# Optimization experiments

Hardware: AMD Instinct MI355X
Metric: run time of the kernel (lower is better)

Reference implementation:

```python
import jax, jax.numpy as jnp
import numpy as np

B, S, H = 2, 2048, 1024
NH, HD = 16, 64  # num heads, head dim


def setup_inputs() -> dict:
    key = jax.random.key(0)
    ks = jax.random.split(key, 8)
    scale = 0.02
    return {
        "hidden_states": jax.random.normal(ks[0], (B, S, H), dtype=jnp.float32),
        "attention_mask": jnp.zeros((B, 1, 1, S), dtype=jnp.float32),
        "Wq": jax.random.normal(ks[1], (H, H), dtype=jnp.float32) * scale,
        "bq": jnp.zeros((H,), dtype=jnp.float32),
        "Wk": jax.random.normal(ks[2], (H, H), dtype=jnp.float32) * scale,
        "bk": jnp.zeros((H,), dtype=jnp.float32),
        "Wv": jax.random.normal(ks[3], (H, H), dtype=jnp.float32) * scale,
        "bv": jnp.zeros((H,), dtype=jnp.float32),
    }


def _split_heads(x):
    # [B,S,H] -> [B,NH,S,HD]
    b, s, _ = x.shape
    return x.reshape(b, s, NH, HD).transpose(0, 2, 1, 3)


def reference(hidden_states, attention_mask, Wq, bq, Wk, bk, Wv, bv):
    q = _split_heads(hidden_states @ Wq.T + bq)
    k = _split_heads(hidden_states @ Wk.T + bk)
    v = _split_heads(hidden_states @ Wv.T + bv)
    # scores: [B,NH,S,S]
    scores = jnp.einsum("bhqd,bhkd->bhqk", q, k) / jnp.sqrt(jnp.float32(HD))
    scores = scores + attention_mask
    att = jax.nn.softmax(scores, axis=-1)  # dropout is identity in eval
    ctx = jnp.einsum("bhqk,bhkd->bhqd", att, v)
    # [B,NH,S,HD] -> [B,S,H]
    return ctx.transpose(0, 2, 1, 3).reshape(hidden_states.shape[0], hidden_states.shape[1], NH * HD)
```

## Files before the change

kernel.cpp:

```cpp
#include <hip/hip_runtime.h>
#include <stdint.h>

#define BB 2
#define SS 2048
#define HH 1024
#define NH 16
#define HD 64

#define LOG2E 1.4426950408889634f
#define QSCALE (0.125f * LOG2E)

typedef short bfrag  __attribute__((ext_vector_type(8)));
typedef short bfrag4 __attribute__((ext_vector_type(4)));
typedef float f32x4  __attribute__((ext_vector_type(4)));

__device__ __forceinline__ short f2bf(float f) {
    union { float f; uint32_t u; } v; v.f = f;
    uint32_t r = (v.u + 0x7fffu + ((v.u >> 16) & 1u)) >> 16;
    return (short)r;
}

__device__ __forceinline__ uint32_t pack_bf16(float a, float b) {
#if __has_builtin(__builtin_amdgcn_cvt_pk_bf16_f32)
    auto t = __builtin_amdgcn_cvt_pk_bf16_f32(a, b);
    uint32_t u; __builtin_memcpy(&u, &t, 4);
    return u;
#else
    uint32_t ua = __float_as_uint(a) + 0x8000u;
    uint32_t ub = __float_as_uint(b) + 0x8000u;
    return __builtin_amdgcn_perm(ub, ua, 0x07060302u);
#endif
}

__global__ __launch_bounds__(256) void cvt_all(
    const float* __restrict__ X,  const float* __restrict__ Wq,
    const float* __restrict__ Wk, const float* __restrict__ Wv,
    const float* __restrict__ mask,
    short* __restrict__ Xb, short* __restrict__ Wcat,
    float* __restrict__ maskl)
{
    int i = blockIdx.x * 256 + threadIdx.x;
    if (i >= 1835008) {
        int off = i - 1835008;
        float4 f = ((const float4*)mask)[off];
        f.x *= LOG2E; f.y *= LOG2E; f.z *= LOG2E; f.w *= LOG2E;
        ((float4*)maskl)[off] = f;
        return;
    }
    const float* src; short* dst; int off;
    if (i < 1048576)      { src = X;  dst = Xb;                 off = i; }
    else if (i < 1310720) { src = Wq; dst = Wcat;               off = i - 1048576; }
    else if (i < 1572864) { src = Wk; dst = Wcat + 1048576;     off = i - 1310720; }
    else                  { src = Wv; dst = Wcat + 2097152;     off = i - 1572864; }
    float4 f = ((const float4*)src)[off];
    short4 s;
    s.x = f2bf(f.x); s.y = f2bf(f.y); s.z = f2bf(f.z); s.w = f2bf(f.w);
    ((short4*)dst)[off] = s;
}

__device__ __forceinline__ void gload_lds16(const void* g, void* lds) {
    __builtin_amdgcn_global_load_lds(
        (__attribute__((address_space(1))) void*)(uintptr_t)g,
        (__attribute__((address_space(3))) void*)(uintptr_t)lds,
        16, 0, 0);
}

__global__ __launch_bounds__(256, 3) void qkv_gemm(
    const short* __restrict__ X, const short* __restrict__ Wcat,
    const float* __restrict__ bq, const float* __restrict__ bk, const float* __restrict__ bv,
    short* __restrict__ Qo, short* __restrict__ Ko, short* __restrict__ Vo)
{
    __shared__ __align__(16) short smem[17408];

    const int tid  = threadIdx.x;
    const int wave = tid >> 6, lane = tid & 63;
    const int quad = lane >> 4, l15 = lane & 15;
    const int mTile = blockIdx.y * 128;
    const int nTile = blockIdx.x * 128;
    const int z = nTile >> 10;
    const int nLocT = nTile & 1023;
    const float* bias = (z == 0) ? bq : (z == 1) ? bk : bv;

    f32x4 acc[4][4];
#pragma unroll
    for (int i = 0; i < 4; ++i)
#pragma unroll
        for (int j = 0; j < 4; ++j) acc[i][j] = (f32x4)0.0f;

    const int srow  = lane >> 3;
    const int c_lin = lane & 7;
    const int mBase = (wave >> 1) * 64;
    const int nBase = (wave & 1) * 64;

    for (int k0 = 0; k0 < 1024; k0 += 64) {
        __syncthreads();
#pragma unroll
        for (int i = 0; i < 4; ++i) {
            int row = i * 32 + wave * 8 + srow;
            int cg  = c_lin ^ (row & 7);
            gload_lds16(X + (size_t)(mTile + row) * 1024 + k0 + cg * 8,
                        (char*)smem + i * 4096 + wave * 1024);
            gload_lds16(Wcat + (size_t)(nTile + row) * 1024 + k0 + cg * 8,
                        (char*)smem + 16384 + i * 4096 + wave * 1024);
        }
        __syncthreads();

#pragma unroll
        for (int kt = 0; kt < 2; ++kt) {
            bfrag af[4], bf[4];
#pragma unroll
            for (int t = 0; t < 4; ++t) {
                int arow = mBase + t * 16 + l15;
                int aslot = (kt * 4 + quad) ^ (arow & 7);
                af[t] = *(const bfrag*)((const char*)smem + arow * 128 + aslot * 16);
                int brow = nBase + t * 16 + l15;
                int bslot = (kt * 4 + quad) ^ (brow & 7);
                bf[t] = *(const bfrag*)((const char*)smem + 16384 + brow * 128 + bslot * 16);
            }
#pragma unroll
            for (int mt = 0; mt < 4; ++mt)
#pragma unroll
                for (int ct = 0; ct < 4; ++ct)
                    acc[mt][ct] = __builtin_amdgcn_mfma_f32_16x16x32_bf16(
                        af[mt], bf[ct], acc[mt][ct], 0, 0, 0);
        }
    }

    __syncthreads();
    const int b = mTile >> 11, sBase = mTile & 2047;

    if (z == 2) {
#pragma unroll
        for (int mt = 0; mt < 4; ++mt)
#pragma unroll
            for (int ct = 0; ct < 4; ++ct)
#pragma unroll
                for (int r = 0; r < 4; ++r) {
                    int nl = nBase + ct * 16 + l15;
                    int sl = mBase + mt * 16 + quad * 4 + r;
                    smem[nl * 136 + sl] = f2bf(acc[mt][ct][r] + bias[nLocT + nl]);
                }
        __syncthreads();
#pragma unroll
        for (int p = 0; p < 8; ++p) {
            int nl = p * 16 + (tid >> 4);
            int cg = tid & 15;
            int blk = cg >> 3;
            int c2  = cg & 7;
            int base = blk * 64 + (c2 >> 2) * 32 + (c2 & 3) * 4;
            int2 lo = *(const int2*)(smem + nl * 136 + base);
            int2 hi = *(const int2*)(smem + nl * 136 + base + 16);
            int4 v; v.x = lo.x; v.y = lo.y; v.z = hi.x; v.w = hi.y;
            int ng = nLocT + nl, hh = ng >> 6, d = ng & 63;
            *(int4*)(Vo + ((size_t)(b * 16 + hh) * 64 + d) * 2048 + sBase + cg * 8) = v;
        }
    } else {
        short* Out = (z == 0) ? Qo : Ko;
        float scale = (z == 0) ? QSCALE : 1.0f;
#pragma unroll
        for (int mt = 0; mt < 4; ++mt)
#pragma unroll
            for (int ct = 0; ct < 4; ++ct)
#pragma unroll
                for (int r = 0; r < 4; ++r) {
                    int ml = mBase + mt * 16 + quad * 4 + r;
                    int nl = nBase + ct * 16 + l15;
                    smem[ml * 136 + nl] = f2bf((acc[mt][ct][r] + bias[nLocT + nl]) * scale);
                }
        __syncthreads();
#pragma unroll
        for (int p = 0; p < 8; ++p) {
            int ml = p * 16 + (tid >> 4);
            int c  = tid & 15;
            bfrag v8 = *(const bfrag*)(smem + ml * 136 + c * 8);
            int s  = sBase + ml;
            int nl = nLocT + c * 8, hh = nl >> 6, d = nl & 63;
            *(bfrag*)(Out + (((size_t)(b * 16 + hh) << 11) + s) * 64 + d) = v8;
        }
    }
}

__global__ __launch_bounds__(256, 4) void attn_kernel(
    const short* __restrict__ Qb, const short* __restrict__ Kb, const short* __restrict__ Vb,
    const float* __restrict__ maskl, float* __restrict__ out)
{
    __shared__ __align__(16) char smem[32768];

    const int tid  = threadIdx.x;
    const int wave = tid >> 6, lane = tid & 63;
    const int quad = lane >> 4, l15 = lane & 15;
    const int bh = blockIdx.y, b = bh >> 4, h = bh & 15;
    const int qBase = blockIdx.x * 64 + wave * 16;

    int ksrc[2], vsrc[2];
#pragma unroll
    for (int i = 0; i < 2; ++i) {
        int ci = wave * 128 + i * 64 + lane;
        int r = ci >> 3, c = ci & 7;
        int cs = (c ^ (r & 7)) * 16;
        ksrc[i] = r * 128  + cs;
        vsrc[i] = r * 4096 + cs;
    }
    const char* kBase = (const char*)(Kb + (size_t)bh * SS * HD);
    const char* vBase = (const char*)(Vb + (size_t)bh * HD * SS);
    const char* mSrc  = (const char*)(maskl + b * SS) + quad * 16;

    const short* Qp = Qb + ((size_t)bh * SS + qBase) * HD;
    bfrag qf[2];
#pragma unroll
    for (int kt = 0; kt < 2; ++kt)
        qf[kt] = *(const bfrag*)(Qp + (size_t)l15 * HD + kt * 32 + quad * 8);

    int kAddr[2];
#pragma unroll
    for (int kt = 0; kt < 2; ++kt)
        kAddr[kt] = l15 * 128 + (((kt * 4 + quad) ^ (l15 & 7)) * 16);
    int vAddr[2];
#pragma unroll
    for (int g = 0; g < 2; ++g)
        vAddr[g] = 8192 + l15 * 128 + (((g * 4 + quad) ^ (l15 & 7)) * 16);

    const f32x4 z4 = (f32x4)0.0f;
    const bfrag4 ones = {0x3F80, 0x3F80, 0x3F80, 0x3F80};

    f32x4 oacc[4], ol = z4;
#pragma unroll
    for (int dt = 0; dt < 4; ++dt) oacc[dt] = z4;

#pragma unroll
    for (int i = 0; i < 2; ++i) {
        gload_lds16(kBase + ksrc[i], smem + wave * 2048 + i * 1024);
        gload_lds16(vBase + vsrc[i], smem + 8192 + wave * 2048 + i * 1024);
    }

    auto astep = [&](int CUR, int NXT, int jn, int pref) {
        __syncthreads();
        if (pref) {
#pragma unroll
            for (int i = 0; i < 2; ++i) {
                gload_lds16(kBase + jn * 8192 + ksrc[i], smem + NXT + wave * 2048 + i * 1024);
                gload_lds16(vBase + jn * 128  + vsrc[i], smem + NXT + 8192 + wave * 2048 + i * 1024);
            }
        }

        f32x4 mvl[4];
#pragma unroll
        for (int ct = 0; ct < 4; ++ct)
            mvl[ct] = *(const f32x4*)(mSrc + ct * 64);
        mSrc += 256;

        f32x4 s[4];
#pragma unroll
        for (int ct = 0; ct < 4; ++ct) {
            bfrag kf0 = *(const bfrag*)(smem + CUR + kAddr[0] + ct * 2048);
            bfrag kf1 = *(const bfrag*)(smem + CUR + kAddr[1] + ct * 2048);
            s[ct] = __builtin_amdgcn_mfma_f32_16x16x32_bf16(kf0, qf[0], mvl[ct], 0, 0, 0);
            s[ct] = __builtin_amdgcn_mfma_f32_16x16x32_bf16(kf1, qf[1], s[ct],   0, 0, 0);
        }

        bfrag4 pf[4];
#pragma unroll
        for (int ct = 0; ct < 4; ++ct) {
            float e0 = __builtin_amdgcn_exp2f(s[ct][0]);
            float e1 = __builtin_amdgcn_exp2f(s[ct][1]);
            float e2 = __builtin_amdgcn_exp2f(s[ct][2]);
            float e3 = __builtin_amdgcn_exp2f(s[ct][3]);
            union { uint32_t u[2]; bfrag4 v; } cvt;
            cvt.u[0] = pack_bf16(e0, e1);
            cvt.u[1] = pack_bf16(e2, e3);
            pf[ct] = cvt.v;
        }

#pragma unroll
        for (int dt = 0; dt < 4; ++dt) {
#pragma unroll
            for (int g = 0; g < 2; ++g) {
                bfrag v = *(const bfrag*)(smem + CUR + vAddr[g] + dt * 2048);
                bfrag4 vlo = __builtin_shufflevector(v, v, 0, 1, 2, 3);
                bfrag4 vhi = __builtin_shufflevector(v, v, 4, 5, 6, 7);
                oacc[dt] = __builtin_amdgcn_mfma_f32_16x16x16bf16_1k(pf[2 * g],     vlo, oacc[dt], 0, 0, 0);
                oacc[dt] = __builtin_amdgcn_mfma_f32_16x16x16bf16_1k(pf[2 * g + 1], vhi, oacc[dt], 0, 0, 0);
            }
        }
#pragma unroll
        for (int ct = 0; ct < 4; ++ct)
            ol = __builtin_amdgcn_mfma_f32_16x16x16bf16_1k(pf[ct], ones, ol, 0, 0, 0);
    };

    for (int jj = 0; jj < 16; ++jj) {
        astep(0,     16384, 2 * jj + 1, 1);
        astep(16384, 0,     2 * jj + 2, jj < 15);
    }

#pragma unroll
    for (int r = 0; r < 4; ++r) {
        float linv = 1.0f / ol[r];
        int qrow = qBase + quad * 4 + r;
#pragma unroll
        for (int dt = 0; dt < 4; ++dt)
            out[((size_t)(b * SS + qrow)) * HH + h * 64 + dt * 16 + l15] =
                oacc[dt][r] * linv;
    }
}

extern "C" void kernel_launch(void* const* d_in, const int* in_sizes, int n_in,
                              void* d_out, int out_size, void* d_ws, size_t ws_size,
                              hipStream_t stream) {
    const float* hs   = (const float*)d_in[0];
    const float* mask = (const float*)d_in[1];
    const float* Wq   = (const float*)d_in[2];
    const float* bq   = (const float*)d_in[3];
    const float* Wk   = (const float*)d_in[4];
    const float* bk   = (const float*)d_in[5];
    const float* Wv   = (const float*)d_in[6];
    const float* bv   = (const float*)d_in[7];
    float* out = (float*)d_out;

    char* ws = (char*)d_ws;
    short* Xb    = (short*)(ws);
    short* Wcat  = (short*)(ws + (8ull  << 20));
    short* Qb    = (short*)(ws + (14ull << 20));
    short* Kb    = (short*)(ws + (22ull << 20));
    short* Vb    = (short*)(ws + (30ull << 20));
    float* maskl = (float*)(ws + (38ull << 20));

    cvt_all<<<7172, 256, 0, stream>>>(hs, Wq, Wk, Wv, mask, Xb, Wcat, maskl);

    qkv_gemm<<<dim3(24, 32), 256, 0, stream>>>(Xb, Wcat, bq, bk, bv, Qb, Kb, Vb);

    attn_kernel<<<dim3(SS / 64, BB * NH), 256, 0, stream>>>(Qb, Kb, Vb, maskl, out);
}
```

Before: 168.5 us.

## Process 32 query rows per wave and remap blocks by head for locality

Each wave in the attention kernel now handles two 16-row query fragments, so every K and V tile loaded from LDS is reused across twice as many query rows. The block tile grows from 64 to 128 queries, and the grid becomes a 1D launch of 512 blocks. Block IDs are swizzled so that consecutive blocks map to different (batch, head) pairs, which is meant to spread K/V reads across cache or XCD partitions. Register pressure roughly doubles, so launch bounds drop from 4 to 2 blocks per SIMD, and the grid is half as large, both of which reduce occupancy.

```diff
diff --git a/kernel.cpp b/kernel.cpp
--- a/kernel.cpp
+++ b/kernel.cpp
@@ -180,7 +180,7 @@
     }
 }
 
-__global__ __launch_bounds__(256, 4) void attn_kernel(
+__global__ __launch_bounds__(256, 2) void attn_kernel(
     const short* __restrict__ Qb, const short* __restrict__ Kb, const short* __restrict__ Vb,
     const float* __restrict__ maskl, float* __restrict__ out)
 {
@@ -189,8 +189,13 @@
     const int tid  = threadIdx.x;
     const int wave = tid >> 6, lane = tid & 63;
     const int quad = lane >> 4, l15 = lane & 15;
-    const int bh = blockIdx.y, b = bh >> 4, h = bh & 15;
-    const int qBase = blockIdx.x * 64 + wave * 16;
+
+    const int id = blockIdx.x;
+    const int slot = id >> 3;
+    const int bh = ((id & 7) << 2) | (slot & 3);
+    const int qt = slot >> 2;
+    const int b  = bh >> 4, h = bh & 15;
+    const int qBase = qt * 128 + wave * 32;
 
     int ksrc[2], vsrc[2];
 #pragma unroll
@@ -206,10 +211,12 @@
     const char* mSrc  = (const char*)(maskl + b * SS) + quad * 16;
 
     const short* Qp = Qb + ((size_t)bh * SS + qBase) * HD;
-    bfrag qf[2];
-#pragma unroll
-    for (int kt = 0; kt < 2; ++kt)
-        qf[kt] = *(const bfrag*)(Qp + (size_t)l15 * HD + kt * 32 + quad * 8);
+    bfrag qf[2][2];
+#pragma unroll
+    for (int hf = 0; hf < 2; ++hf)
+#pragma unroll
+        for (int kt = 0; kt < 2; ++kt)
+            qf[hf][kt] = *(const bfrag*)(Qp + (size_t)(hf * 16 + l15) * HD + kt * 32 + quad * 8);
 
     int kAddr[2];
 #pragma unroll
@@ -223,9 +230,13 @@
     const f32x4 z4 = (f32x4)0.0f;
     const bfrag4 ones = {0x3F80, 0x3F80, 0x3F80, 0x3F80};
 
-    f32x4 oacc[4], ol = z4;
-#pragma unroll
-    for (int dt = 0; dt < 4; ++dt) oacc[dt] = z4;
+    f32x4 oacc[2][4], ol[2];
+#pragma unroll
+    for (int hf = 0; hf < 2; ++hf) {
+        ol[hf] = z4;
+#pragma unroll
+        for (int dt = 0; dt < 4; ++dt) oacc[hf][dt] = z4;
+    }
 
 #pragma unroll
     for (int i = 0; i < 2; ++i) {
@@ -249,26 +260,27 @@
             mvl[ct] = *(const f32x4*)(mSrc + ct * 64);
         mSrc += 256;
 
-        f32x4 s[4];
+        f32x4 s0[4], s1[4];
 #pragma unroll
         for (int ct = 0; ct < 4; ++ct) {
             bfrag kf0 = *(const bfrag*)(smem + CUR + kAddr[0] + ct * 2048);
             bfrag kf1 = *(const bfrag*)(smem + CUR + kAddr[1] + ct * 2048);
-            s[ct] = __builtin_amdgcn_mfma_f32_16x16x32_bf16(kf0, qf[0], mvl[ct], 0, 0, 0);
-            s[ct] = __builtin_amdgcn_mfma_f32_16x16x32_bf16(kf1, qf[1], s[ct],   0, 0, 0);
-        }
-
-        bfrag4 pf[4];
+            s0[ct] = __builtin_amdgcn_mfma_f32_16x16x32_bf16(kf0, qf[0][0], mvl[ct], 0, 0, 0);
+            s0[ct] = __builtin_amdgcn_mfma_f32_16x16x32_bf16(kf1, qf[0][1], s0[ct],  0, 0, 0);
+            s1[ct] = __builtin_amdgcn_mfma_f32_16x16x32_bf16(kf0, qf[1][0], mvl[ct], 0, 0, 0);
+            s1[ct] = __builtin_amdgcn_mfma_f32_16x16x32_bf16(kf1, qf[1][1], s1[ct],  0, 0, 0);
+        }
+
+        bfrag4 pf0[4], pf1[4];
 #pragma unroll
         for (int ct = 0; ct < 4; ++ct) {
-            float e0 = __builtin_amdgcn_exp2f(s[ct][0]);
-            float e1 = __builtin_amdgcn_exp2f(s[ct][1]);
-            float e2 = __builtin_amdgcn_exp2f(s[ct][2]);
-            float e3 = __builtin_amdgcn_exp2f(s[ct][3]);
             union { uint32_t u[2]; bfrag4 v; } cvt;
-            cvt.u[0] = pack_bf16(e0, e1);
-            cvt.u[1] = pack_bf16(e2, e3);
-            pf[ct] = cvt.v;
+            cvt.u[0] = pack_bf16(__builtin_amdgcn_exp2f(s0[ct][0]), __builtin_amdgcn_exp2f(s0[ct][1]));
+            cvt.u[1] = pack_bf16(__builtin_amdgcn_exp2f(s0[ct][2]), __builtin_amdgcn_exp2f(s0[ct][3]));
+            pf0[ct] = cvt.v;
+            cvt.u[0] = pack_bf16(__builtin_amdgcn_exp2f(s1[ct][0]), __builtin_amdgcn_exp2f(s1[ct][1]));
+            cvt.u[1] = pack_bf16(__builtin_amdgcn_exp2f(s1[ct][2]), __builtin_amdgcn_exp2f(s1[ct][3]));
+            pf1[ct] = cvt.v;
         }
 
 #pragma unroll
@@ -278,13 +290,17 @@
                 bfrag v = *(const bfrag*)(smem + CUR + vAddr[g] + dt * 2048);
                 bfrag4 vlo = __builtin_shufflevector(v, v, 0, 1, 2, 3);
                 bfrag4 vhi = __builtin_shufflevector(v, v, 4, 5, 6, 7);
-                oacc[dt] = __builtin_amdgcn_mfma_f32_16x16x16bf16_1k(pf[2 * g],     vlo, oacc[dt], 0, 0, 0);
-                oacc[dt] = __builtin_amdgcn_mfma_f32_16x16x16bf16_1k(pf[2 * g + 1], vhi, oacc[dt], 0, 0, 0);
+                oacc[0][dt] = __builtin_amdgcn_mfma_f32_16x16x16bf16_1k(pf0[2 * g],     vlo, oacc[0][dt], 0, 0, 0);
+                oacc[0][dt] = __builtin_amdgcn_mfma_f32_16x16x16bf16_1k(pf0[2 * g + 1], vhi, oacc[0][dt], 0, 0, 0);
+                oacc[1][dt] = __builtin_amdgcn_mfma_f32_16x16x16bf16_1k(pf1[2 * g],     vlo, oacc[1][dt], 0, 0, 0);
+                oacc[1][dt] = __builtin_amdgcn_mfma_f32_16x16x16bf16_1k(pf1[2 * g + 1], vhi, oacc[1][dt], 0, 0, 0);
             }
         }
 #pragma unroll
-        for (int ct = 0; ct < 4; ++ct)
-            ol = __builtin_amdgcn_mfma_f32_16x16x16bf16_1k(pf[ct], ones, ol, 0, 0, 0);
+        for (int ct = 0; ct < 4; ++ct) {
+            ol[0] = __builtin_amdgcn_mfma_f32_16x16x16bf16_1k(pf0[ct], ones, ol[0], 0, 0, 0);
+            ol[1] = __builtin_amdgcn_mfma_f32_16x16x16bf16_1k(pf1[ct], ones, ol[1], 0, 0, 0);
+        }
     };
 
     for (int jj = 0; jj < 16; ++jj) {
@@ -293,13 +309,16 @@
     }
 
 #pragma unroll
-    for (int r = 0; r < 4; ++r) {
-        float linv = 1.0f / ol[r];
-        int qrow = qBase + quad * 4 + r;
-#pragma unroll
-        for (int dt = 0; dt < 4; ++dt)
-            out[((size_t)(b * SS + qrow)) * HH + h * 64 + dt * 16 + l15] =
-                oacc[dt][r] * linv;
+    for (int hf = 0; hf < 2; ++hf) {
+#pragma unroll
+        for (int r = 0; r < 4; ++r) {
+            float linv = 1.0f / ol[hf][r];
+            int qrow = qBase + hf * 16 + quad * 4 + r;
+#pragma unroll
+            for (int dt = 0; dt < 4; ++dt)
+                out[((size_t)(b * SS + qrow)) * HH + h * 64 + dt * 16 + l15] =
+                    oacc[hf][dt][r] * linv;
+        }
     }
 }
 
@@ -328,5 +347,5 @@
 
     qkv_gemm<<<dim3(24, 32), 256, 0, stream>>>(Xb, Wcat, bq, bk, bv, Qb, Kb, Vb);
 
-    attn_kernel<<<dim3(SS / 64, BB * NH), 256, 0, stream>>>(Qb, Kb, Vb, maskl, out);
-}
+    attn_kernel<<<512, 256, 0, stream>>>(Qb, Kb, Vb, maskl, out);
+}
```

Measured after the change: 165.6 us. About the same (-1.7%).
